# Performance work log

Measured on AMD Instinct MI355X. Metric: run time of the kernel, lower is better.

The kernel has to match this reference:

```python
import jax, jax.numpy as jnp
import numpy as np

B, L, V, D = 8, 2048, 1024, 512  # batch, seq (max_len), vocab_size (input feat), embedding_dim

def setup_inputs() -> dict:
    key = jax.random.key(0)
    kx, kq, kk, kv = jax.random.split(key, 4)
    scale = 1.0 / np.sqrt(V)
    return {
        "x": jax.random.normal(kx, (B, L, V), dtype=jnp.float32),
        "Wq": jax.random.uniform(kq, (D, V), dtype=jnp.float32, minval=-scale, maxval=scale),
        "Wk": jax.random.uniform(kk, (D, V), dtype=jnp.float32, minval=-scale, maxval=scale),
        "Wv": jax.random.uniform(kv, (D, V), dtype=jnp.float32, minval=-scale, maxval=scale),
    }

def reference(x, Wq, Wk, Wv):
    # nn.Linear without bias: y = x @ W.T
    q = jnp.einsum('blv,dv->bld', x, Wq)
    k = jnp.einsum('blv,dv->bld', x, Wk)
    v = jnp.einsum('blv,dv->bld', x, Wv)
    scores = jnp.einsum('bqd,bkd->bqk', q, k) / jnp.sqrt(jnp.float32(D))
    attn = jax.nn.softmax(scores, axis=2)
    return jnp.einsum('bqk,bkd->bqd', attn, v)
```

## Files before the change

kernel.cpp:

```cpp
#include <hip/hip_runtime.h>
#include <cstdint>
#include <cstddef>


typedef __attribute__((ext_vector_type(8))) __bf16 bf16x8;
typedef __attribute__((ext_vector_type(4))) float f32x4;
typedef __attribute__((ext_vector_type(4))) unsigned short ushort4v;

__device__ __forceinline__ unsigned short f2bf(float f) {
  unsigned u = __float_as_uint(f);
  return (unsigned short)((u + 0x7fffu + ((u >> 16) & 1u)) >> 16);
}

__device__ __forceinline__ void async_load16(const unsigned short* g, unsigned short* l) {
  __builtin_amdgcn_global_load_lds(
      (__attribute__((address_space(1))) void*)(g),
      (__attribute__((address_space(3))) void*)(l), 16, 0, 0);
}

__global__ __launch_bounds__(256) void cvt_f32_bf16(const float* __restrict__ src,
                                                    unsigned short* __restrict__ dst) {
  int i = (blockIdx.x * 256 + threadIdx.x) * 4;
  float4 v = *(const float4*)(src + i);
  ushort4v o;
  o.x = f2bf(v.x); o.y = f2bf(v.y); o.z = f2bf(v.z); o.w = f2bf(v.w);
  *(ushort4v*)(dst + i) = o;
}

__global__ __launch_bounds__(256) void cvt_w3(const float* __restrict__ a,
                                              const float* __restrict__ b,
                                              const float* __restrict__ c,
                                              unsigned short* __restrict__ dst) {
  int bx = blockIdx.x;
  const float* src = (bx < 512) ? a : (bx < 1024) ? b : c;
  int seg = (bx < 512) ? 0 : (bx < 1024) ? 1 : 2;
  int i = ((bx & 511) * 256 + threadIdx.x) * 4;
  float4 v = *(const float4*)(src + i);
  ushort4v o;
  o.x = f2bf(v.x); o.y = f2bf(v.y); o.z = f2bf(v.z); o.w = f2bf(v.w);
  *(ushort4v*)(dst + seg * 524288 + i) = o;
}

__global__ __launch_bounds__(256) void zero_f32(float* __restrict__ p) {
  int i = (blockIdx.x * 256 + threadIdx.x) * 4;
  *(float4*)(p + i) = make_float4(0.f, 0.f, 0.f, 0.f);
}

template <int MODE>
__global__ __launch_bounds__(256) void gemm_bt(
    const unsigned short* __restrict__ A, long long lda, long long strideA,
    const unsigned short* __restrict__ B, long long ldb, long long strideB,
    unsigned short* __restrict__ C, long long ldc, long long strideC,
    int K, float scale,
    unsigned short* __restrict__ vout,
    float* __restrict__ rowsum) {
  __shared__ unsigned short sA[128 * 64];
  __shared__ unsigned short sB[128 * 64];

  const int tid = threadIdx.x;
  const int lane = tid & 63, wid = tid >> 6;
  const int wm = wid & 1, wn = wid >> 1;
  const int l15 = lane & 15, lq = lane >> 4;

  A += (size_t)blockIdx.z * strideA + (size_t)blockIdx.y * 128 * lda;
  B += (size_t)blockIdx.z * strideB + (size_t)blockIdx.x * 128 * ldb;

  f32x4 acc[4][4] = {};

  for (int k0 = 0; k0 < K; k0 += 64) {
    __syncthreads();
    #pragma unroll
    for (int p = 0; p < 4; ++p) {
      int u = p * 256 + tid;
      int r = u >> 3;
      int cs = (u & 7) ^ (r & 7);
      async_load16(&A[(size_t)r * lda + k0 + cs * 8], &sA[u * 8]);
      async_load16(&B[(size_t)r * ldb + k0 + cs * 8], &sB[u * 8]);
    }
    __syncthreads();

    #pragma unroll
    for (int kk = 0; kk < 2; ++kk) {
      bf16x8 aF[4], bF[4];
      int cb = kk * 4 + lq;
      #pragma unroll
      for (int i = 0; i < 4; ++i) {
        int rA = wm * 64 + i * 16 + l15;
        aF[i] = *(const bf16x8*)&sA[(rA * 8 + (cb ^ (rA & 7))) * 8];
        int rB = wn * 64 + i * 16 + l15;
        bF[i] = *(const bf16x8*)&sB[(rB * 8 + (cb ^ (rB & 7))) * 8];
      }
      #pragma unroll
      for (int mt = 0; mt < 4; ++mt)
        #pragma unroll
        for (int nt = 0; nt < 4; ++nt)
          acc[mt][nt] = __builtin_amdgcn_mfma_f32_16x16x32_bf16(
              aF[mt], bF[nt], acc[mt][nt], 0, 0, 0);
    }
  }

  if (MODE == 1) {
    if (blockIdx.x < 8) {
      unsigned short* Cc = C + (size_t)blockIdx.y * 128 * ldc + (size_t)blockIdx.x * 128;
      #pragma unroll
      for (int mt = 0; mt < 4; ++mt)
        #pragma unroll
        for (int nt = 0; nt < 4; ++nt) {
          int row = wm * 64 + mt * 16 + lq * 4;
          int col = wn * 64 + nt * 16 + l15;
          #pragma unroll
          for (int r2 = 0; r2 < 4; ++r2)
            Cc[(size_t)(row + r2) * ldc + col] = f2bf(acc[mt][nt][r2]);
        }
    } else {
      int nvx = blockIdx.x - 8;
      #pragma unroll
      for (int mt = 0; mt < 4; ++mt)
        #pragma unroll
        for (int nt = 0; nt < 4; ++nt) {
          int grow = blockIdx.y * 128 + wm * 64 + mt * 16 + lq * 4;
          int b = grow >> 11, l = grow & 2047;
          int d = nvx * 128 + wn * 64 + nt * 16 + l15;
          ushort4v o;
          o.x = f2bf(acc[mt][nt][0]); o.y = f2bf(acc[mt][nt][1]);
          o.z = f2bf(acc[mt][nt][2]); o.w = f2bf(acc[mt][nt][3]);
          *(ushort4v*)&vout[(size_t)b * 1048576 + (size_t)d * 2048 + l] = o;
        }
    }
  } else {
    unsigned short* Cc = C + (size_t)blockIdx.z * strideC +
                         (size_t)blockIdx.y * 128 * ldc + (size_t)blockIdx.x * 128;
    #pragma unroll
    for (int mt = 0; mt < 4; ++mt) {
      float rs0 = 0.f, rs1 = 0.f, rs2 = 0.f, rs3 = 0.f;
      #pragma unroll
      for (int nt = 0; nt < 4; ++nt) {
        #pragma unroll
        for (int r2 = 0; r2 < 4; ++r2)
          acc[mt][nt][r2] = __expf(acc[mt][nt][r2] * scale);
        rs0 += acc[mt][nt][0]; rs1 += acc[mt][nt][1];
        rs2 += acc[mt][nt][2]; rs3 += acc[mt][nt][3];
      }
      #pragma unroll
      for (int off = 1; off < 16; off <<= 1) {
        rs0 += __shfl_xor(rs0, off, 64); rs1 += __shfl_xor(rs1, off, 64);
        rs2 += __shfl_xor(rs2, off, 64); rs3 += __shfl_xor(rs3, off, 64);
      }
      if (l15 == 0) {
        int gr = blockIdx.z * 2048 + blockIdx.y * 128 + wm * 64 + mt * 16 + lq * 4;
        atomicAdd(&rowsum[gr], rs0); atomicAdd(&rowsum[gr + 1], rs1);
        atomicAdd(&rowsum[gr + 2], rs2); atomicAdd(&rowsum[gr + 3], rs3);
      }
      #pragma unroll
      for (int nt = 0; nt < 4; ++nt) {
        int row = wm * 64 + mt * 16 + lq * 4;
        int col = wn * 64 + nt * 16 + l15;
        #pragma unroll
        for (int r2 = 0; r2 < 4; ++r2)
          Cc[(size_t)(row + r2) * ldc + col] = f2bf(acc[mt][nt][r2]);
      }
    }
  }
}

__global__ __launch_bounds__(256) void gemm_pv(
    const unsigned short* __restrict__ P, const unsigned short* __restrict__ vT,
    const float* __restrict__ rowsum, float* __restrict__ out) {
  __shared__ unsigned short sA[64 * 64];
  __shared__ unsigned short sB[128 * 64];
  const int tid = threadIdx.x;
  const int lane = tid & 63, wid = tid >> 6;
  const int l15 = lane & 15, lq = lane >> 4;
  const int b = blockIdx.z;
  const int m0 = blockIdx.y * 64;
  const int n0 = blockIdx.x * 128;
  const unsigned short* A = P + (size_t)b * 4194304 + (size_t)m0 * 2048;
  const unsigned short* B = vT + (size_t)b * 1048576 + (size_t)n0 * 2048;

  f32x4 acc[4][2] = {};

  for (int k0 = 0; k0 < 2048; k0 += 64) {
    __syncthreads();
    #pragma unroll
    for (int p = 0; p < 2; ++p) {
      int u = p * 256 + tid;
      int r = u >> 3, cs = (u & 7) ^ (r & 7);
      async_load16(&A[(size_t)r * 2048 + k0 + cs * 8], &sA[u * 8]);
    }
    #pragma unroll
    for (int p = 0; p < 4; ++p) {
      int u = p * 256 + tid;
      int r = u >> 3, cs = (u & 7) ^ (r & 7);
      async_load16(&B[(size_t)r * 2048 + k0 + cs * 8], &sB[u * 8]);
    }
    __syncthreads();

    #pragma unroll
    for (int kk = 0; kk < 2; ++kk) {
      bf16x8 aF[4], bF[2];
      int cb = kk * 4 + lq;
      #pragma unroll
      for (int i = 0; i < 4; ++i) {
        int rA = i * 16 + l15;
        aF[i] = *(const bf16x8*)&sA[(rA * 8 + (cb ^ (rA & 7))) * 8];
      }
      #pragma unroll
      for (int j = 0; j < 2; ++j) {
        int rB = wid * 32 + j * 16 + l15;
        bF[j] = *(const bf16x8*)&sB[(rB * 8 + (cb ^ (rB & 7))) * 8];
      }
      #pragma unroll
      for (int mt = 0; mt < 4; ++mt)
        #pragma unroll
        for (int nt = 0; nt < 2; ++nt)
          acc[mt][nt] = __builtin_amdgcn_mfma_f32_16x16x32_bf16(
              aF[mt], bF[nt], acc[mt][nt], 0, 0, 0);
    }
  }

  #pragma unroll
  for (int mt = 0; mt < 4; ++mt) {
    int gr = m0 + mt * 16 + lq * 4;
    float4 rs4 = *(const float4*)&rowsum[(size_t)b * 2048 + gr];
    float inv[4] = {1.f / rs4.x, 1.f / rs4.y, 1.f / rs4.z, 1.f / rs4.w};
    #pragma unroll
    for (int nt = 0; nt < 2; ++nt) {
      int col = n0 + wid * 32 + nt * 16 + l15;
      #pragma unroll
      for (int r2 = 0; r2 < 4; ++r2)
        out[((size_t)b * 2048 + gr + r2) * 512 + col] = acc[mt][nt][r2] * inv[r2];
    }
  }
}

extern "C" void kernel_launch(void* const* d_in, const int* in_sizes, int n_in,
                              void* d_out, int out_size, void* d_ws, size_t ws_size,
                              hipStream_t stream) {
  const float* x  = (const float*)d_in[0];
  const float* Wq = (const float*)d_in[1];
  const float* Wk = (const float*)d_in[2];
  const float* Wv = (const float*)d_in[3];
  float* out = (float*)d_out;
  char* ws = (char*)d_ws;

  unsigned short* xb = (unsigned short*)ws;
  unsigned short* S  = (unsigned short*)ws;
  unsigned short* wf = (unsigned short*)(ws + 33554432);
  unsigned short* qk = (unsigned short*)(ws + 67108864);
  unsigned short* vT = (unsigned short*)(ws + 100663296);
  float* rowsum = (float*)(ws + 117440512);

  const float rsqrtD = 0.044194173824159216f;

  hipLaunchKernelGGL(cvt_f32_bf16, dim3(16384), dim3(256), 0, stream, x, xb);
  hipLaunchKernelGGL(cvt_w3, dim3(1536), dim3(256), 0, stream, Wq, Wk, Wv, wf);
  hipLaunchKernelGGL(zero_f32, dim3(16), dim3(256), 0, stream, rowsum);

  hipLaunchKernelGGL((gemm_bt<1>), dim3(12, 128, 1), dim3(256), 0, stream,
                     xb, 1024LL, 0LL, wf, 1024LL, 0LL,
                     qk, 1024LL, 0LL, 1024, 1.0f, vT, (float*)nullptr);

  hipLaunchKernelGGL((gemm_bt<2>), dim3(16, 16, 8), dim3(256), 0, stream,
                     qk, 1024LL, 2097152LL, qk + 512, 1024LL, 2097152LL,
                     S, 2048LL, 4194304LL, 512, rsqrtD,
                     (unsigned short*)nullptr, rowsum);

  hipLaunchKernelGGL(gemm_pv, dim3(4, 32, 8), dim3(256), 0, stream,
                     S, vT, rowsum, out);

  (void)in_sizes; (void)n_in; (void)out_size; (void)ws_size;
}
```

Before: 295.9 us.

## Use 32x32x16 MFMA for QKV and PV GEMMs, enlarge PV tile, fold zeroing

The QKV projection and P·V GEMMs switch from 16x16x32 to 32x32x16 bf16 MFMA with 2x2 accumulator tiles per wave, which cuts LDS fragment reads per MFMA. The PV kernel grows its M tile from 64 to 128 rows with a 2x2 wave layout, halving the grid and the number of times V is reloaded. The rowsum zeroing kernel is folded into the weight-conversion kernel to save a launch. The larger PV tile halves the block count, which may reduce occupancy and latency hiding.

```diff
diff --git a/kernel.cpp b/kernel.cpp
--- a/kernel.cpp
+++ b/kernel.cpp
@@ -5,6 +5,7 @@
 
 typedef __attribute__((ext_vector_type(8))) __bf16 bf16x8;
 typedef __attribute__((ext_vector_type(4))) float f32x4;
+typedef __attribute__((ext_vector_type(16))) float f32x16;
 typedef __attribute__((ext_vector_type(4))) unsigned short ushort4v;
 
 __device__ __forceinline__ unsigned short f2bf(float f) {
@@ -30,8 +31,13 @@
 __global__ __launch_bounds__(256) void cvt_w3(const float* __restrict__ a,
                                               const float* __restrict__ b,
                                               const float* __restrict__ c,
-                                              unsigned short* __restrict__ dst) {
+                                              unsigned short* __restrict__ dst,
+                                              float* __restrict__ rowsum) {
   int bx = blockIdx.x;
+  if (bx < 16) {
+    int j = (bx * 256 + threadIdx.x) * 4;
+    *(float4*)(rowsum + j) = make_float4(0.f, 0.f, 0.f, 0.f);
+  }
   const float* src = (bx < 512) ? a : (bx < 1024) ? b : c;
   int seg = (bx < 512) ? 0 : (bx < 1024) ? 1 : 2;
   int i = ((bx & 511) * 256 + threadIdx.x) * 4;
@@ -41,41 +47,113 @@
   *(ushort4v*)(dst + seg * 524288 + i) = o;
 }
 
-__global__ __launch_bounds__(256) void zero_f32(float* __restrict__ p) {
-  int i = (blockIdx.x * 256 + threadIdx.x) * 4;
-  *(float4*)(p + i) = make_float4(0.f, 0.f, 0.f, 0.f);
-}
-
-template <int MODE>
-__global__ __launch_bounds__(256) void gemm_bt(
-    const unsigned short* __restrict__ A, long long lda, long long strideA,
-    const unsigned short* __restrict__ B, long long ldb, long long strideB,
-    unsigned short* __restrict__ C, long long ldc, long long strideC,
-    int K, float scale,
-    unsigned short* __restrict__ vout,
+__global__ __launch_bounds__(256) void gemm_qkv(
+    const unsigned short* __restrict__ A,
+    const unsigned short* __restrict__ Bw,
+    unsigned short* __restrict__ qk,
+    unsigned short* __restrict__ vT) {
+  __shared__ unsigned short sA[128 * 64];
+  __shared__ unsigned short sB[128 * 64];
+  const int tid = threadIdx.x;
+  const int lane = tid & 63, wid = tid >> 6;
+  const int wm = wid & 1, wn = wid >> 1;
+  const int l31 = lane & 31, half = lane >> 5;
+
+  A += (size_t)blockIdx.y * 128 * 1024;
+  Bw += (size_t)blockIdx.x * 128 * 1024;
+
+  f32x16 acc[2][2] = {};
+
+  for (int k0 = 0; k0 < 1024; k0 += 64) {
+    __syncthreads();
+    #pragma unroll
+    for (int p = 0; p < 4; ++p) {
+      int u = p * 256 + tid;
+      int r = u >> 3, cs = (u & 7) ^ (r & 7);
+      async_load16(&A[(size_t)r * 1024 + k0 + cs * 8], &sA[u * 8]);
+      async_load16(&Bw[(size_t)r * 1024 + k0 + cs * 8], &sB[u * 8]);
+    }
+    __syncthreads();
+
+    #pragma unroll
+    for (int ks = 0; ks < 4; ++ks) {
+      int cb = ks * 2 + half;
+      bf16x8 aF[2], bF[2];
+      #pragma unroll
+      for (int i = 0; i < 2; ++i) {
+        int rA = wm * 64 + i * 32 + l31;
+        aF[i] = *(const bf16x8*)&sA[(rA * 8 + (cb ^ (rA & 7))) * 8];
+        int rB = wn * 64 + i * 32 + l31;
+        bF[i] = *(const bf16x8*)&sB[(rB * 8 + (cb ^ (rB & 7))) * 8];
+      }
+      #pragma unroll
+      for (int mt = 0; mt < 2; ++mt)
+        #pragma unroll
+        for (int nt = 0; nt < 2; ++nt)
+          acc[mt][nt] = __builtin_amdgcn_mfma_f32_32x32x16_bf16(
+              aF[mt], bF[nt], acc[mt][nt], 0, 0, 0);
+    }
+  }
+
+  if (blockIdx.x < 8) {
+    unsigned short* Cc = qk + (size_t)blockIdx.y * 128 * 1024 + (size_t)blockIdx.x * 128;
+    #pragma unroll
+    for (int mt = 0; mt < 2; ++mt)
+      #pragma unroll
+      for (int nt = 0; nt < 2; ++nt) {
+        int col = wn * 64 + nt * 32 + l31;
+        #pragma unroll
+        for (int q = 0; q < 4; ++q) {
+          int row = wm * 64 + mt * 32 + half * 4 + q * 8;
+          #pragma unroll
+          for (int r2 = 0; r2 < 4; ++r2)
+            Cc[(size_t)(row + r2) * 1024 + col] = f2bf(acc[mt][nt][q * 4 + r2]);
+        }
+      }
+  } else {
+    int nvx = blockIdx.x - 8;
+    #pragma unroll
+    for (int mt = 0; mt < 2; ++mt)
+      #pragma unroll
+      for (int nt = 0; nt < 2; ++nt) {
+        int d = nvx * 128 + wn * 64 + nt * 32 + l31;
+        #pragma unroll
+        for (int q = 0; q < 4; ++q) {
+          int grow = blockIdx.y * 128 + wm * 64 + mt * 32 + half * 4 + q * 8;
+          int b = grow >> 11, l = grow & 2047;
+          ushort4v o;
+          o.x = f2bf(acc[mt][nt][q * 4 + 0]); o.y = f2bf(acc[mt][nt][q * 4 + 1]);
+          o.z = f2bf(acc[mt][nt][q * 4 + 2]); o.w = f2bf(acc[mt][nt][q * 4 + 3]);
+          *(ushort4v*)&vT[(size_t)b * 1048576 + (size_t)d * 2048 + l] = o;
+        }
+      }
+  }
+}
+
+__global__ __launch_bounds__(256) void gemm_exp(
+    const unsigned short* __restrict__ qk,
+    unsigned short* __restrict__ S, float scale,
     float* __restrict__ rowsum) {
   __shared__ unsigned short sA[128 * 64];
   __shared__ unsigned short sB[128 * 64];
-
   const int tid = threadIdx.x;
   const int lane = tid & 63, wid = tid >> 6;
   const int wm = wid & 1, wn = wid >> 1;
   const int l15 = lane & 15, lq = lane >> 4;
 
-  A += (size_t)blockIdx.z * strideA + (size_t)blockIdx.y * 128 * lda;
-  B += (size_t)blockIdx.z * strideB + (size_t)blockIdx.x * 128 * ldb;
+  const unsigned short* A = qk + (size_t)blockIdx.z * 2097152 + (size_t)blockIdx.y * 128 * 1024;
+  const unsigned short* Bk = qk + 512 + (size_t)blockIdx.z * 2097152 + (size_t)blockIdx.x * 128 * 1024;
 
   f32x4 acc[4][4] = {};
 
-  for (int k0 = 0; k0 < K; k0 += 64) {
+  for (int k0 = 0; k0 < 512; k0 += 64) {
     __syncthreads();
     #pragma unroll
     for (int p = 0; p < 4; ++p) {
       int u = p * 256 + tid;
-      int r = u >> 3;
-      int cs = (u & 7) ^ (r & 7);
-      async_load16(&A[(size_t)r * lda + k0 + cs * 8], &sA[u * 8]);
-      async_load16(&B[(size_t)r * ldb + k0 + cs * 8], &sB[u * 8]);
+      int r = u >> 3, cs = (u & 7) ^ (r & 7);
+      async_load16(&A[(size_t)r * 1024 + k0 + cs * 8], &sA[u * 8]);
+      async_load16(&Bk[(size_t)r * 1024 + k0 + cs * 8], &sB[u * 8]);
     }
     __syncthreads();
 
@@ -99,66 +177,36 @@
     }
   }
 
-  if (MODE == 1) {
-    if (blockIdx.x < 8) {
-      unsigned short* Cc = C + (size_t)blockIdx.y * 128 * ldc + (size_t)blockIdx.x * 128;
-      #pragma unroll
-      for (int mt = 0; mt < 4; ++mt)
-        #pragma unroll
-        for (int nt = 0; nt < 4; ++nt) {
-          int row = wm * 64 + mt * 16 + lq * 4;
-          int col = wn * 64 + nt * 16 + l15;
-          #pragma unroll
-          for (int r2 = 0; r2 < 4; ++r2)
-            Cc[(size_t)(row + r2) * ldc + col] = f2bf(acc[mt][nt][r2]);
-        }
-    } else {
-      int nvx = blockIdx.x - 8;
-      #pragma unroll
-      for (int mt = 0; mt < 4; ++mt)
-        #pragma unroll
-        for (int nt = 0; nt < 4; ++nt) {
-          int grow = blockIdx.y * 128 + wm * 64 + mt * 16 + lq * 4;
-          int b = grow >> 11, l = grow & 2047;
-          int d = nvx * 128 + wn * 64 + nt * 16 + l15;
-          ushort4v o;
-          o.x = f2bf(acc[mt][nt][0]); o.y = f2bf(acc[mt][nt][1]);
-          o.z = f2bf(acc[mt][nt][2]); o.w = f2bf(acc[mt][nt][3]);
-          *(ushort4v*)&vout[(size_t)b * 1048576 + (size_t)d * 2048 + l] = o;
-        }
-    }
-  } else {
-    unsigned short* Cc = C + (size_t)blockIdx.z * strideC +
-                         (size_t)blockIdx.y * 128 * ldc + (size_t)blockIdx.x * 128;
-    #pragma unroll
-    for (int mt = 0; mt < 4; ++mt) {
-      float rs0 = 0.f, rs1 = 0.f, rs2 = 0.f, rs3 = 0.f;
-      #pragma unroll
-      for (int nt = 0; nt < 4; ++nt) {
-        #pragma unroll
-        for (int r2 = 0; r2 < 4; ++r2)
-          acc[mt][nt][r2] = __expf(acc[mt][nt][r2] * scale);
-        rs0 += acc[mt][nt][0]; rs1 += acc[mt][nt][1];
-        rs2 += acc[mt][nt][2]; rs3 += acc[mt][nt][3];
-      }
-      #pragma unroll
-      for (int off = 1; off < 16; off <<= 1) {
-        rs0 += __shfl_xor(rs0, off, 64); rs1 += __shfl_xor(rs1, off, 64);
-        rs2 += __shfl_xor(rs2, off, 64); rs3 += __shfl_xor(rs3, off, 64);
-      }
-      if (l15 == 0) {
-        int gr = blockIdx.z * 2048 + blockIdx.y * 128 + wm * 64 + mt * 16 + lq * 4;
-        atomicAdd(&rowsum[gr], rs0); atomicAdd(&rowsum[gr + 1], rs1);
-        atomicAdd(&rowsum[gr + 2], rs2); atomicAdd(&rowsum[gr + 3], rs3);
-      }
-      #pragma unroll
-      for (int nt = 0; nt < 4; ++nt) {
-        int row = wm * 64 + mt * 16 + lq * 4;
-        int col = wn * 64 + nt * 16 + l15;
-        #pragma unroll
-        for (int r2 = 0; r2 < 4; ++r2)
-          Cc[(size_t)(row + r2) * ldc + col] = f2bf(acc[mt][nt][r2]);
-      }
+  unsigned short* Cc = S + (size_t)blockIdx.z * 4194304 +
+                       (size_t)blockIdx.y * 128 * 2048 + (size_t)blockIdx.x * 128;
+  #pragma unroll
+  for (int mt = 0; mt < 4; ++mt) {
+    float rs0 = 0.f, rs1 = 0.f, rs2 = 0.f, rs3 = 0.f;
+    #pragma unroll
+    for (int nt = 0; nt < 4; ++nt) {
+      #pragma unroll
+      for (int r2 = 0; r2 < 4; ++r2)
+        acc[mt][nt][r2] = __expf(acc[mt][nt][r2] * scale);
+      rs0 += acc[mt][nt][0]; rs1 += acc[mt][nt][1];
+      rs2 += acc[mt][nt][2]; rs3 += acc[mt][nt][3];
+    }
+    #pragma unroll
+    for (int off = 1; off < 16; off <<= 1) {
+      rs0 += __shfl_xor(rs0, off, 64); rs1 += __shfl_xor(rs1, off, 64);
+      rs2 += __shfl_xor(rs2, off, 64); rs3 += __shfl_xor(rs3, off, 64);
+    }
+    if (l15 == 0) {
+      int gr = blockIdx.z * 2048 + blockIdx.y * 128 + wm * 64 + mt * 16 + lq * 4;
+      atomicAdd(&rowsum[gr], rs0); atomicAdd(&rowsum[gr + 1], rs1);
+      atomicAdd(&rowsum[gr + 2], rs2); atomicAdd(&rowsum[gr + 3], rs3);
+    }
+    #pragma unroll
+    for (int nt = 0; nt < 4; ++nt) {
+      int row = wm * 64 + mt * 16 + lq * 4;
+      int col = wn * 64 + nt * 16 + l15;
+      #pragma unroll
+      for (int r2 = 0; r2 < 4; ++r2)
+        Cc[(size_t)(row + r2) * 2048 + col] = f2bf(acc[mt][nt][r2]);
     }
   }
 }
@@ -166,69 +214,67 @@
 __global__ __launch_bounds__(256) void gemm_pv(
     const unsigned short* __restrict__ P, const unsigned short* __restrict__ vT,
     const float* __restrict__ rowsum, float* __restrict__ out) {
-  __shared__ unsigned short sA[64 * 64];
+  __shared__ unsigned short sA[128 * 64];
   __shared__ unsigned short sB[128 * 64];
   const int tid = threadIdx.x;
   const int lane = tid & 63, wid = tid >> 6;
-  const int l15 = lane & 15, lq = lane >> 4;
+  const int wm = wid & 1, wn = wid >> 1;
+  const int l31 = lane & 31, half = lane >> 5;
   const int b = blockIdx.z;
-  const int m0 = blockIdx.y * 64;
-  const int n0 = blockIdx.x * 128;
+  const int m0 = blockIdx.y * 128, n0 = blockIdx.x * 128;
   const unsigned short* A = P + (size_t)b * 4194304 + (size_t)m0 * 2048;
-  const unsigned short* B = vT + (size_t)b * 1048576 + (size_t)n0 * 2048;
-
-  f32x4 acc[4][2] = {};
+  const unsigned short* Bv = vT + (size_t)b * 1048576 + (size_t)n0 * 2048;
+
+  f32x16 acc[2][2] = {};
 
   for (int k0 = 0; k0 < 2048; k0 += 64) {
     __syncthreads();
     #pragma unroll
-    for (int p = 0; p < 2; ++p) {
+    for (int p = 0; p < 4; ++p) {
       int u = p * 256 + tid;
       int r = u >> 3, cs = (u & 7) ^ (r & 7);
       async_load16(&A[(size_t)r * 2048 + k0 + cs * 8], &sA[u * 8]);
-    }
-    #pragma unroll
-    for (int p = 0; p < 4; ++p) {
-      int u = p * 256 + tid;
-      int r = u >> 3, cs = (u & 7) ^ (r & 7);
-      async_load16(&B[(size_t)r * 2048 + k0 + cs * 8], &sB[u * 8]);
-    }
-    __syncthreads();
-
-    #pragma unroll
-    for (int kk = 0; kk < 2; ++kk) {
-      bf16x8 aF[4], bF[2];
-      int cb = kk * 4 + lq;
-      #pragma unroll
-      for (int i = 0; i < 4; ++i) {
-        int rA = i * 16 + l15;
+      async_load16(&Bv[(size_t)r * 2048 + k0 + cs * 8], &sB[u * 8]);
+    }
+    __syncthreads();
+
+    #pragma unroll
+    for (int ks = 0; ks < 4; ++ks) {
+      int cb = ks * 2 + half;
+      bf16x8 aF[2], bF[2];
+      #pragma unroll
+      for (int i = 0; i < 2; ++i) {
+        int rA = wm * 64 + i * 32 + l31;
         aF[i] = *(const bf16x8*)&sA[(rA * 8 + (cb ^ (rA & 7))) * 8];
-      }
-      #pragma unroll
-      for (int j = 0; j < 2; ++j) {
-        int rB = wid * 32 + j * 16 + l15;
-        bF[j] = *(const bf16x8*)&sB[(rB * 8 + (cb ^ (rB & 7))) * 8];
-      }
-      #pragma unroll
-      for (int mt = 0; mt < 4; ++mt)
+        int rB = wn * 64 + i * 32 + l31;
+        bF[i] = *(const bf16x8*)&sB[(rB * 8 + (cb ^ (rB & 7))) * 8];
+      }
+      #pragma unroll
+      for (int mt = 0; mt < 2; ++mt)
         #pragma unroll
         for (int nt = 0; nt < 2; ++nt)
-          acc[mt][nt] = __builtin_amdgcn_mfma_f32_16x16x32_bf16(
+          acc[mt][nt] = __builtin_amdgcn_mfma_f32_32x32x16_bf16(
               aF[mt], bF[nt], acc[mt][nt], 0, 0, 0);
     }
   }
 
   #pragma unroll
-  for (int mt = 0; mt < 4; ++mt) {
-    int gr = m0 + mt * 16 + lq * 4;
-    float4 rs4 = *(const float4*)&rowsum[(size_t)b * 2048 + gr];
-    float inv[4] = {1.f / rs4.x, 1.f / rs4.y, 1.f / rs4.z, 1.f / rs4.w};
-    #pragma unroll
-    for (int nt = 0; nt < 2; ++nt) {
-      int col = n0 + wid * 32 + nt * 16 + l15;
-      #pragma unroll
-      for (int r2 = 0; r2 < 4; ++r2)
-        out[((size_t)b * 2048 + gr + r2) * 512 + col] = acc[mt][nt][r2] * inv[r2];
+  for (int mt = 0; mt < 2; ++mt) {
+    #pragma unroll
+    for (int q = 0; q < 4; ++q) {
+      int row = m0 + wm * 64 + mt * 32 + half * 4 + q * 8;
+      float4 rs = *(const float4*)&rowsum[(size_t)b * 2048 + row];
+      float inv0 = __builtin_amdgcn_rcpf(rs.x), inv1 = __builtin_amdgcn_rcpf(rs.y);
+      float inv2 = __builtin_amdgcn_rcpf(rs.z), inv3 = __builtin_amdgcn_rcpf(rs.w);
+      #pragma unroll
+      for (int nt = 0; nt < 2; ++nt) {
+        int col = n0 + wn * 64 + nt * 32 + l31;
+        float* op = out + ((size_t)b * 2048 + row) * 512 + col;
+        op[0]    = acc[mt][nt][q * 4 + 0] * inv0;
+        op[512]  = acc[mt][nt][q * 4 + 1] * inv1;
+        op[1024] = acc[mt][nt][q * 4 + 2] * inv2;
+        op[1536] = acc[mt][nt][q * 4 + 3] * inv3;
+      }
     }
   }
 }
@@ -253,20 +299,14 @@
   const float rsqrtD = 0.044194173824159216f;
 
   hipLaunchKernelGGL(cvt_f32_bf16, dim3(16384), dim3(256), 0, stream, x, xb);
-  hipLaunchKernelGGL(cvt_w3, dim3(1536), dim3(256), 0, stream, Wq, Wk, Wv, wf);
-  hipLaunchKernelGGL(zero_f32, dim3(16), dim3(256), 0, stream, rowsum);
-
-  hipLaunchKernelGGL((gemm_bt<1>), dim3(12, 128, 1), dim3(256), 0, stream,
-                     xb, 1024LL, 0LL, wf, 1024LL, 0LL,
-                     qk, 1024LL, 0LL, 1024, 1.0f, vT, (float*)nullptr);
-
-  hipLaunchKernelGGL((gemm_bt<2>), dim3(16, 16, 8), dim3(256), 0, stream,
-                     qk, 1024LL, 2097152LL, qk + 512, 1024LL, 2097152LL,
-                     S, 2048LL, 4194304LL, 512, rsqrtD,
-                     (unsigned short*)nullptr, rowsum);
-
-  hipLaunchKernelGGL(gemm_pv, dim3(4, 32, 8), dim3(256), 0, stream,
-                     S, vT, rowsum, out);
+  hipLaunchKernelGGL(cvt_w3, dim3(1536), dim3(256), 0, stream, Wq, Wk, Wv, wf, rowsum);
+
+  hipLaunchKernelGGL(gemm_qkv, dim3(12, 128, 1), dim3(256), 0, stream, xb, wf, qk, vT);
+
+  hipLaunchKernelGGL(gemm_exp, dim3(16, 16, 8), dim3(256), 0, stream,
+                     qk, S, rsqrtD, rowsum);
+
+  hipLaunchKernelGGL(gemm_pv, dim3(4, 16, 8), dim3(256), 0, stream, S, vT, rowsum, out);
 
   (void)in_sizes; (void)n_in; (void)out_size; (void)ws_size;
 }
```

After: 292.6 us. About the same (-1.1%).
